# Kernel optimization log

Hardware: AMD Instinct MI355X
Metric: run time of the kernel (lower is better)

## Reference

```python
import jax, jax.numpy as jnp
import numpy as np

B, S, D = 8, 2048, 1024


def setup_inputs() -> dict:
    key = jax.random.key(0)
    ks = jax.random.split(key, 9)
    scale = 1.0 / np.sqrt(D)
    inp = {
        "query": jax.random.normal(ks[0], (B, S, D), dtype=jnp.float32),
        "key": jax.random.normal(ks[1], (B, S, D), dtype=jnp.float32),
        "value": jax.random.normal(ks[2], (B, S, D), dtype=jnp.float32),
        # causal boolean mask, broadcast over batch; True = keep, False = -inf
        "mask": jnp.tril(jnp.ones((S, S), dtype=bool)),
        "Wq": jax.random.normal(ks[3], (D, D), dtype=jnp.float32) * scale,
        "bq": jax.random.normal(ks[4], (D,), dtype=jnp.float32) * 0.02,
        "Wk": jax.random.normal(ks[5], (D, D), dtype=jnp.float32) * scale,
        "bk": jax.random.normal(ks[6], (D,), dtype=jnp.float32) * 0.02,
        "Wv": jax.random.normal(ks[7], (D, D), dtype=jnp.float32) * scale,
        "bv": jax.random.normal(ks[8], (D,), dtype=jnp.float32) * 0.02,
    }
    return inp


def reference(query, key, value, mask, Wq, bq, Wk, bk, Wv, bv):
    dk = Wq.shape[1]
    # linear projections: nn.Linear stores weight as [out,in]; here W is [in,out]
    q = jnp.einsum("bsd,de->bse", query, Wq) + bq
    k = jnp.einsum("bsd,de->bse", key, Wk) + bk
    v = jnp.einsum("bsd,de->bse", value, Wv) + bv
    # scaled dot-product scores [B, S, S]
    scores = jnp.einsum("bqd,bkd->bqk", q, k) / jnp.sqrt(jnp.asarray(dk, q.dtype))
    scores = jnp.where(mask, scores, jnp.asarray(-jnp.inf, scores.dtype))
    attn = jax.nn.softmax(scores, axis=-1)
    return jnp.einsum("bqk,bkd->bqd", attn, v)
```

## Files before the change

### kernel.cpp

```cpp
#include <hip/hip_runtime.h>

#define BB 8
#define SS 2048
#define DD 1024
#define BK 32
#define TSZ (128 * BK)

typedef unsigned short u16;
typedef __bf16 bf16x8 __attribute__((ext_vector_type(8)));
typedef float f32x4 __attribute__((ext_vector_type(4)));

__device__ __forceinline__ u16 f2bf(float f) {
  unsigned int u = __builtin_bit_cast(unsigned int, f);
  u += 0x7fffu + ((u >> 16) & 1u);
  return (u16)(u >> 16);
}
__device__ __forceinline__ float bf2f(u16 h) {
  unsigned int u = ((unsigned int)h) << 16;
  return __builtin_bit_cast(float, u);
}

__device__ __forceinline__ void gl2lds16(const u16* g, u16* l) {
  __builtin_amdgcn_global_load_lds(
      (const __attribute__((address_space(1))) unsigned int*)g,
      (__attribute__((address_space(3))) unsigned int*)l, 16, 0, 0);
}

__device__ __forceinline__ void stage_tile(const u16* gbase, size_t gstride,
                                           u16* lds, int wave, int lane) {
#pragma unroll
  for (int r = 0; r < 2; r++) {
    int rowblk = r * 64 + wave * 16;
    int row = rowblk + (lane >> 2);
    int col = (lane & 3) * 8;
    gl2lds16(gbase + (size_t)row * gstride + col, lds + rowblk * BK);
  }
}

__device__ __forceinline__ void mfma_tile(const u16* As, const u16* Bs, int wm, int wn,
                                          int quad, int l16, f32x4 (&acc)[4][4]) {
  bf16x8 a[4], b[4];
#pragma unroll
  for (int i = 0; i < 4; i++)
    a[i] = *reinterpret_cast<const bf16x8*>(&As[(wm + i * 16 + l16) * BK + quad * 8]);
#pragma unroll
  for (int j = 0; j < 4; j++)
    b[j] = *reinterpret_cast<const bf16x8*>(&Bs[(wn + j * 16 + l16) * BK + quad * 8]);
#pragma unroll
  for (int i = 0; i < 4; i++)
#pragma unroll
    for (int j = 0; j < 4; j++)
      acc[i][j] = __builtin_amdgcn_mfma_f32_16x16x32_bf16(a[i], b[j], acc[i][j], 0, 0, 0);
}

__global__ void prep(const float* __restrict__ q, const float* __restrict__ k,
                     const float* __restrict__ v, u16* __restrict__ Xall,
                     const float* __restrict__ Wq, const float* __restrict__ Wk,
                     const float* __restrict__ Wv, u16* __restrict__ Wall) {
  __shared__ u16 t[32][33];
  int id = blockIdx.x;
  if (id < 24576) {
    int z = id >> 13;
    int chunk = id & 8191;
    const float* x = (z == 0) ? q : (z == 1) ? k : v;
    u16* y = Xall + (size_t)z * (BB * SS * DD);
    size_t i = (size_t)chunk * 256 + threadIdx.x;
    const float4* s = (const float4*)x;
    float4 a = s[2 * i], b = s[2 * i + 1];
    uint4 p;
    p.x = (unsigned)f2bf(a.x) | ((unsigned)f2bf(a.y) << 16);
    p.y = (unsigned)f2bf(a.z) | ((unsigned)f2bf(a.w) << 16);
    p.z = (unsigned)f2bf(b.x) | ((unsigned)f2bf(b.y) << 16);
    p.w = (unsigned)f2bf(b.z) | ((unsigned)f2bf(b.w) << 16);
    ((uint4*)y)[i] = p;
  } else {
    int tt = id - 24576;
    int z = tt >> 10, t2 = tt & 1023;
    const float* W = (z == 0) ? Wq : (z == 1) ? Wk : Wv;
    u16* Wt = Wall + (size_t)z * (DD * DD);
    int n0 = (t2 & 31) * 32, k0 = (t2 >> 5) * 32;
    int tx = threadIdx.x & 31, ty = threadIdx.x >> 5;
#pragma unroll
    for (int i = 0; i < 32; i += 8)
      t[ty + i][tx] = f2bf(W[(size_t)(k0 + ty + i) * DD + n0 + tx]);
    __syncthreads();
#pragma unroll
    for (int i = 0; i < 32; i += 8)
      Wt[(size_t)(n0 + ty + i) * DD + k0 + tx] = t[tx][ty + i];
  }
}

__global__ void proj_gemm(const u16* __restrict__ Xall, const u16* __restrict__ Wall,
                          const float* __restrict__ bq, const float* __restrict__ bk,
                          const float* __restrict__ bv, u16* __restrict__ QK,
                          u16* __restrict__ Vt) {
  __shared__ __align__(16) u16 As[2 * TSZ];
  __shared__ __align__(16) u16 Bs[2 * TSZ];
  int id = blockIdx.x;
  int z = id >> 10, rem = id & 1023;
  int r = rem & 7, j = rem >> 3;
  int bn = j & 7, bm = ((j >> 3) << 3) | r;
  const u16* Xb = Xall + (size_t)z * (BB * SS * DD);
  const u16* Wt = Wall + (size_t)z * (DD * DD);
  const float* bias = (z == 0) ? bq : (z == 1) ? bk : bv;
  int m0 = bm * 128, n0 = bn * 128;
  int tid = threadIdx.x;
  int lane = tid & 63, wave = tid >> 6;
  int wm = (wave >> 1) * 64, wn = (wave & 1) * 64;
  int quad = lane >> 4, l16 = lane & 15;

  const u16* Abase = (z < 2) ? (Xb + (size_t)m0 * DD) : (Wt + (size_t)n0 * DD);
  const u16* Bbase = (z < 2) ? (Wt + (size_t)n0 * DD) : (Xb + (size_t)m0 * DD);

  f32x4 acc[4][4];
  f32x4 zz = {0.f, 0.f, 0.f, 0.f};
#pragma unroll
  for (int i = 0; i < 4; i++)
#pragma unroll
    for (int jj = 0; jj < 4; jj++) acc[i][jj] = zz;

  for (int k0 = 0; k0 < DD; k0 += 2 * BK) {
    __syncthreads();
    stage_tile(Abase + k0, DD, As, wave, lane);
    stage_tile(Abase + k0 + BK, DD, As + TSZ, wave, lane);
    stage_tile(Bbase + k0, DD, Bs, wave, lane);
    stage_tile(Bbase + k0 + BK, DD, Bs + TSZ, wave, lane);
    __syncthreads();
    mfma_tile(As, Bs, wm, wn, quad, l16, acc);
    mfma_tile(As + TSZ, Bs + TSZ, wm, wn, quad, l16, acc);
  }
  if (z < 2) {
    u16* Out = QK + (size_t)z * (BB * SS * DD);
#pragma unroll
    for (int i = 0; i < 4; i++) {
#pragma unroll
      for (int rr = 0; rr < 4; rr++) {
        int row = m0 + wm + i * 16 + quad * 4 + rr;
#pragma unroll
        for (int jj = 0; jj < 4; jj++) {
          int col = n0 + wn + jj * 16 + l16;
          Out[(size_t)row * DD + col] = f2bf(acc[i][jj][rr] + bias[col]);
        }
      }
    }
  } else {
    int b = m0 >> 11, s0 = m0 & 2047;
#pragma unroll
    for (int i = 0; i < 4; i++) {
#pragma unroll
      for (int rr = 0; rr < 4; rr++) {
        int d = n0 + wm + i * 16 + quad * 4 + rr;
        float bd = bias[d];
#pragma unroll
        for (int jj = 0; jj < 4; jj++) {
          int s = s0 + wn + jj * 16 + l16;
          Vt[((size_t)b * DD + d) * SS + s] = f2bf(acc[i][jj][rr] + bd);
        }
      }
    }
  }
}

__global__ void scores_gemm(const u16* __restrict__ Q, const u16* __restrict__ Kp,
                            u16* __restrict__ Sc) {
  __shared__ __align__(16) u16 As[2 * TSZ];
  __shared__ __align__(16) u16 Bs[2 * TSZ];
  int id = blockIdx.x;
  int b = id & 7, t = id >> 3;
  int bm = (int)((sqrtf(8.f * t + 1.f) - 1.f) * 0.5f);
  while ((bm + 1) * (bm + 2) / 2 <= t) bm++;
  while (bm * (bm + 1) / 2 > t) bm--;
  int bn = t - bm * (bm + 1) / 2;

  const u16* Qb = Q + (size_t)b * SS * DD;
  const u16* Kb = Kp + (size_t)b * SS * DD;
  u16* Sb = Sc + (size_t)b * SS * SS;
  int m0 = bm * 128, n0 = bn * 128;
  int tid = threadIdx.x;
  int lane = tid & 63, wave = tid >> 6;
  int wm = (wave >> 1) * 64, wn = (wave & 1) * 64;
  int quad = lane >> 4, l16 = lane & 15;

  f32x4 acc[4][4];
  f32x4 z = {0.f, 0.f, 0.f, 0.f};
#pragma unroll
  for (int i = 0; i < 4; i++)
#pragma unroll
    for (int jj = 0; jj < 4; jj++) acc[i][jj] = z;

  for (int k0 = 0; k0 < DD; k0 += 2 * BK) {
    __syncthreads();
    stage_tile(Qb + (size_t)m0 * DD + k0, DD, As, wave, lane);
    stage_tile(Qb + (size_t)m0 * DD + k0 + BK, DD, As + TSZ, wave, lane);
    stage_tile(Kb + (size_t)n0 * DD + k0, DD, Bs, wave, lane);
    stage_tile(Kb + (size_t)n0 * DD + k0 + BK, DD, Bs + TSZ, wave, lane);
    __syncthreads();
    mfma_tile(As, Bs, wm, wn, quad, l16, acc);
    mfma_tile(As + TSZ, Bs + TSZ, wm, wn, quad, l16, acc);
  }
#pragma unroll
  for (int i = 0; i < 4; i++) {
#pragma unroll
    for (int rr = 0; rr < 4; rr++) {
      int gi = m0 + wm + i * 16 + quad * 4 + rr;
#pragma unroll
      for (int jj = 0; jj < 4; jj++) {
        int gj = n0 + wn + jj * 16 + l16;
        if (gj <= gi) Sb[(size_t)gi * SS + gj] = f2bf(acc[i][jj][rr] * 0.03125f);
      }
    }
  }
}

__global__ void softmax_causal(const u16* __restrict__ Sc, u16* __restrict__ P) {
  int i = blockIdx.x, b = blockIdx.y;
  const u16* srow = Sc + ((size_t)b * SS + i) * SS;
  u16* prow = P + ((size_t)b * SS + i) * SS;
  int n = i + 1;
  int nceil = ((i >> 7) + 1) << 7;
  int tid = threadIdx.x;
  int lane = tid & 63, wave = tid >> 6;
  __shared__ float sm[4];
  __shared__ float ssum[4];

  int j0 = tid * 8;
  bool act = j0 < nceil;
  float v[8];
  float mx = -3.0e38f;
  if (act) {
    uint4 raw = ((const uint4*)srow)[tid];
    unsigned w[4] = {raw.x, raw.y, raw.z, raw.w};
#pragma unroll
    for (int u = 0; u < 8; u++) {
      u16 h = (u16)((w[u >> 1] >> ((u & 1) * 16)) & 0xffffu);
      v[u] = (j0 + u < n) ? bf2f(h) : -3.0e38f;
      mx = fmaxf(mx, v[u]);
    }
  } else {
#pragma unroll
    for (int u = 0; u < 8; u++) v[u] = -3.0e38f;
  }
#pragma unroll
  for (int off = 32; off > 0; off >>= 1) mx = fmaxf(mx, __shfl_down(mx, off, 64));
  if (lane == 0) sm[wave] = mx;
  __syncthreads();
  mx = fmaxf(fmaxf(sm[0], sm[1]), fmaxf(sm[2], sm[3]));

  float e[8];
  float sum = 0.f;
#pragma unroll
  for (int u = 0; u < 8; u++) {
    e[u] = __expf(v[u] - mx);
    sum += e[u];
  }
#pragma unroll
  for (int off = 32; off > 0; off >>= 1) sum += __shfl_down(sum, off, 64);
  if (lane == 0) ssum[wave] = sum;
  __syncthreads();
  sum = ssum[0] + ssum[1] + ssum[2] + ssum[3];
  float inv = 1.0f / sum;
  if (act) {
    uint4 o;
    unsigned* ow = (unsigned*)&o;
#pragma unroll
    for (int u = 0; u < 4; u++) {
      u16 lo = f2bf(e[2 * u] * inv);
      u16 hi = f2bf(e[2 * u + 1] * inv);
      ow[u] = (unsigned)lo | ((unsigned)hi << 16);
    }
    ((uint4*)prow)[tid] = o;
  }
}

__global__ void pv_gemm(const u16* __restrict__ P, const u16* __restrict__ Vt,
                        float* __restrict__ O) {
  __shared__ __align__(16) u16 As[2 * 64 * BK];
  __shared__ __align__(16) u16 Bs[2 * TSZ];
  int id = blockIdx.x;
  int bn = id & 7, q = (id >> 3) & 15, b = id >> 7;
  const u16* Pb = P + (size_t)b * SS * SS;
  const u16* Vb = Vt + (size_t)b * SS * DD;
  float* Ob = O + (size_t)b * SS * DD;
  int n0 = bn * 128;
  int tid = threadIdx.x;
  int lane = tid & 63, wave = tid >> 6;
  int wn = wave * 32;
  int quad = lane >> 4, l16 = lane & 15;

#pragma unroll
  for (int phase = 0; phase < 2; phase++) {
    int bm = phase ? (31 - q) : q;
    int m0 = bm * 64;
    f32x4 acc[4][2];
    f32x4 z = {0.f, 0.f, 0.f, 0.f};
#pragma unroll
    for (int i = 0; i < 4; i++)
#pragma unroll
      for (int jj = 0; jj < 2; jj++) acc[i][jj] = z;

    int kmax = (bm + 1) * 64;
    for (int k0 = 0; k0 < kmax; k0 += 2 * BK) {
      __syncthreads();
#pragma unroll
      for (int sub = 0; sub < 2; sub++) {
        int row = wave * 16 + (lane >> 2);
        int col = (lane & 3) * 8;
        gl2lds16(Pb + (size_t)(m0 + row) * SS + k0 + sub * BK + col,
                 As + sub * 64 * BK + wave * 16 * BK);
      }
      stage_tile(Vb + (size_t)n0 * SS + k0, SS, Bs, wave, lane);
      stage_tile(Vb + (size_t)n0 * SS + k0 + BK, SS, Bs + TSZ, wave, lane);
      __syncthreads();
#pragma unroll
      for (int sub = 0; sub < 2; sub++) {
        const u16* Asub = As + sub * 64 * BK;
        const u16* Bsub = Bs + sub * TSZ;
        bf16x8 a[4], bb[2];
#pragma unroll
        for (int i = 0; i < 4; i++)
          a[i] = *reinterpret_cast<const bf16x8*>(&Asub[(i * 16 + l16) * BK + quad * 8]);
#pragma unroll
        for (int jj = 0; jj < 2; jj++)
          bb[jj] = *reinterpret_cast<const bf16x8*>(&Bsub[(wn + jj * 16 + l16) * BK + quad * 8]);
#pragma unroll
        for (int i = 0; i < 4; i++)
#pragma unroll
          for (int jj = 0; jj < 2; jj++)
            acc[i][jj] = __builtin_amdgcn_mfma_f32_16x16x32_bf16(a[i], bb[jj], acc[i][jj], 0, 0, 0);
      }
    }
#pragma unroll
    for (int i = 0; i < 4; i++) {
#pragma unroll
      for (int rr = 0; rr < 4; rr++) {
        int row = m0 + i * 16 + quad * 4 + rr;
#pragma unroll
        for (int jj = 0; jj < 2; jj++) {
          int col = n0 + wn + jj * 16 + l16;
          Ob[(size_t)row * DD + col] = acc[i][jj][rr];
        }
      }
    }
  }
}

extern "C" void kernel_launch(void* const* d_in, const int* in_sizes, int n_in,
                              void* d_out, int out_size, void* d_ws, size_t ws_size,
                              hipStream_t stream) {
  const float* query = (const float*)d_in[0];
  const float* key_ = (const float*)d_in[1];
  const float* value = (const float*)d_in[2];
  const float* Wq = (const float*)d_in[4];
  const float* bq = (const float*)d_in[5];
  const float* Wk = (const float*)d_in[6];
  const float* bk = (const float*)d_in[7];
  const float* Wv = (const float*)d_in[8];
  const float* bv = (const float*)d_in[9];
  float* out = (float*)d_out;
  char* ws = (char*)d_ws;

  const size_t MB = 1048576ull;
  u16* Xall = (u16*)(ws + 0);
  u16* QK   = (u16*)(ws + 96 * MB);
  u16* Qb   = (u16*)(ws + 96 * MB);
  u16* Kb   = (u16*)(ws + 128 * MB);
  u16* Vt   = (u16*)(ws + 160 * MB);
  u16* Wall = (u16*)(ws + 192 * MB);
  u16* Sc   = (u16*)(ws + 32 * MB);
  u16* P    = (u16*)(ws + 96 * MB);

  dim3 blk(256, 1, 1);
  prep<<<dim3(27648, 1, 1), blk, 0, stream>>>(query, key_, value, Xall, Wq, Wk, Wv, Wall);
  proj_gemm<<<dim3(3072, 1, 1), blk, 0, stream>>>(Xall, Wall, bq, bk, bv, QK, Vt);
  scores_gemm<<<dim3(1088, 1, 1), blk, 0, stream>>>(Qb, Kb, Sc);
  softmax_causal<<<dim3(2048, 8, 1), blk, 0, stream>>>(Sc, P);
  pv_gemm<<<dim3(1024, 1, 1), blk, 0, stream>>>(P, Vt, out);
}
```

Baseline: 487.6 us.

## Rewrite projection GEMM with 256x256 tiles, 8 waves and pipelined LDS staging

The projection GEMM moves from 128x128 tiles with 4 waves to 256x256 tiles with 8 waves per block. It uses a deeper asynchronous global-to-LDS prefetch pipeline, throttled with explicit vmcnt waits and split barriers. LDS reads use an XOR swizzle to avoid bank conflicts, and the MFMA phases are interleaved with staging using setprio. The aim is higher operand reuse and less load latency exposed in the dominant GEMM stage, at the cost of more registers and LDS (128KB) and fragile hand-written synchronization.

```diff
diff --git a/kernel.cpp b/kernel.cpp
--- a/kernel.cpp
+++ b/kernel.cpp
@@ -90,70 +90,164 @@
   }
 }
 
-__global__ void proj_gemm(const u16* __restrict__ Xall, const u16* __restrict__ Wall,
-                          const float* __restrict__ bq, const float* __restrict__ bk,
-                          const float* __restrict__ bv, u16* __restrict__ QK,
-                          u16* __restrict__ Vt) {
-  __shared__ __align__(16) u16 As[2 * TSZ];
-  __shared__ __align__(16) u16 Bs[2 * TSZ];
+#define NKT 16
+
+#define LGK0 asm volatile("s_waitcnt lgkmcnt(0)" ::: "memory")
+#define VMW(n) asm volatile("s_waitcnt vmcnt(" #n ")" ::: "memory")
+#define BARF do { __builtin_amdgcn_s_barrier(); asm volatile("" ::: "memory"); } while (0)
+
+template <int I0, int J0>
+__device__ __forceinline__ void quad_mfma(f32x4 (&acc)[8][4], const bf16x8 (&a)[4][2],
+                                          const bf16x8 (&b)[2][2]) {
+#pragma unroll
+  for (int ks = 0; ks < 2; ks++)
+#pragma unroll
+    for (int i = 0; i < 4; i++)
+#pragma unroll
+      for (int jj = 0; jj < 2; jj++)
+        acc[I0 + i][J0 + jj] = __builtin_amdgcn_mfma_f32_16x16x32_bf16(
+            a[i][ks], b[jj][ks], acc[I0 + i][J0 + jj], 0, 0, 0);
+}
+
+__global__ __launch_bounds__(512, 2) void proj_gemm(
+    const u16* __restrict__ Xall, const u16* __restrict__ Wall,
+    const float* __restrict__ bq, const float* __restrict__ bk,
+    const float* __restrict__ bv, u16* __restrict__ QK, u16* __restrict__ Vt) {
+  __shared__ __align__(16) u16 sA[2][2][8192];
+  __shared__ __align__(16) u16 sB[2][2][8192];
   int id = blockIdx.x;
-  int z = id >> 10, rem = id & 1023;
-  int r = rem & 7, j = rem >> 3;
-  int bn = j & 7, bm = ((j >> 3) << 3) | r;
+  int z = id >> 8, rem = id & 255;
+  int r = rem & 7, j0 = rem >> 3;
+  int bw = j0 & 3, bx = (j0 >> 2) * 8 + r;
   const u16* Xb = Xall + (size_t)z * (BB * SS * DD);
   const u16* Wt = Wall + (size_t)z * (DD * DD);
   const float* bias = (z == 0) ? bq : (z == 1) ? bk : bv;
-  int m0 = bm * 128, n0 = bn * 128;
+  const u16* Ab = (z < 2) ? Xb + (size_t)bx * 256 * DD : Wt + (size_t)bw * 256 * DD;
+  const u16* Bb = (z < 2) ? Wt + (size_t)bw * 256 * DD : Xb + (size_t)bx * 256 * DD;
+
   int tid = threadIdx.x;
   int lane = tid & 63, wave = tid >> 6;
-  int wm = (wave >> 1) * 64, wn = (wave & 1) * 64;
-  int quad = lane >> 4, l16 = lane & 15;
-
-  const u16* Abase = (z < 2) ? (Xb + (size_t)m0 * DD) : (Wt + (size_t)n0 * DD);
-  const u16* Bbase = (z < 2) ? (Wt + (size_t)n0 * DD) : (Xb + (size_t)m0 * DD);
-
-  f32x4 acc[4][4];
+  int wrow = wave >> 2, wcol = wave & 3;
+  int quad = lane >> 4, l16 = lane & 15, sw = l16 & 7;
+  int k0off = (quad ^ sw) * 8;
+  int k1off = ((quad + 4) ^ sw) * 8;
+
+  u16* sAf = &sA[0][0][0];
+  u16* sBf = &sB[0][0][0];
+
+  auto stage = [&](int h) {
+    int tt = h >> 2, d = h & 3;
+    u16* l = ((d < 2) ? sBf : sAf) + ((((tt & 1) << 1) | (d & 1)) * 8192);
+    const u16* g = ((d < 2) ? Bb : Ab) + (size_t)((d & 1) * 128) * DD + tt * 64;
+#pragma unroll
+    for (int ii = 0; ii < 2; ii++) {
+      int reg = wave * 2 + ii;
+      int row = reg * 8 + (lane >> 3);
+      int col = ((lane & 7) ^ (lane >> 3)) * 8;
+      gl2lds16(g + (size_t)row * DD + col, l + reg * 512);
+    }
+  };
+
+  f32x4 acc[8][4];
   f32x4 zz = {0.f, 0.f, 0.f, 0.f};
 #pragma unroll
-  for (int i = 0; i < 4; i++)
+  for (int i = 0; i < 8; i++)
 #pragma unroll
     for (int jj = 0; jj < 4; jj++) acc[i][jj] = zz;
 
-  for (int k0 = 0; k0 < DD; k0 += 2 * BK) {
-    __syncthreads();
-    stage_tile(Abase + k0, DD, As, wave, lane);
-    stage_tile(Abase + k0 + BK, DD, As + TSZ, wave, lane);
-    stage_tile(Bbase + k0, DD, Bs, wave, lane);
-    stage_tile(Bbase + k0 + BK, DD, Bs + TSZ, wave, lane);
-    __syncthreads();
-    mfma_tile(As, Bs, wm, wn, quad, l16, acc);
-    mfma_tile(As + TSZ, Bs + TSZ, wm, wn, quad, l16, acc);
-  }
+#pragma unroll
+  for (int h = 0; h < 6; h++) stage(h);
+  VMW(4);
+  BARF;
+
+#pragma unroll 2
+  for (int t = 0; t < NKT; ++t) {
+    int buf = t & 1;
+    const u16* At0 = sAf + (buf * 2 + wrow) * 8192 + l16 * 64 + k0off;
+    const u16* At1 = sAf + (buf * 2 + wrow) * 8192 + l16 * 64 + k1off;
+    const u16* Bt0 = sBf + (buf * 2 + (wcol >> 1)) * 8192 + ((wcol & 1) * 64 + l16) * 64 + k0off;
+    const u16* Bt1 = sBf + (buf * 2 + (wcol >> 1)) * 8192 + ((wcol & 1) * 64 + l16) * 64 + k1off;
+    bf16x8 al[4][2], ah[4][2], bl[2][2], bh[2][2];
+#pragma unroll
+    for (int i = 0; i < 4; i++) {
+      al[i][0] = *reinterpret_cast<const bf16x8*>(At0 + i * 1024);
+      al[i][1] = *reinterpret_cast<const bf16x8*>(At1 + i * 1024);
+    }
+#pragma unroll
+    for (int jj = 0; jj < 2; jj++) {
+      bl[jj][0] = *reinterpret_cast<const bf16x8*>(Bt0 + jj * 1024);
+      bl[jj][1] = *reinterpret_cast<const bf16x8*>(Bt1 + jj * 1024);
+    }
+    if (4 * t + 6 < 4 * NKT) stage(4 * t + 6);
+    __builtin_amdgcn_s_barrier();
+    LGK0;
+    __builtin_amdgcn_s_setprio(1);
+    quad_mfma<0, 0>(acc, al, bl);
+    __builtin_amdgcn_s_setprio(0);
+    BARF;
+#pragma unroll
+    for (int jj = 0; jj < 2; jj++) {
+      bh[jj][0] = *reinterpret_cast<const bf16x8*>(Bt0 + (2 + jj) * 1024);
+      bh[jj][1] = *reinterpret_cast<const bf16x8*>(Bt1 + (2 + jj) * 1024);
+    }
+    if (4 * t + 7 < 4 * NKT) stage(4 * t + 7);
+    __builtin_amdgcn_s_barrier();
+    LGK0;
+    __builtin_amdgcn_s_setprio(1);
+    quad_mfma<0, 2>(acc, al, bh);
+    __builtin_amdgcn_s_setprio(0);
+    BARF;
+#pragma unroll
+    for (int i = 0; i < 4; i++) {
+      ah[i][0] = *reinterpret_cast<const bf16x8*>(At0 + (4 + i) * 1024);
+      ah[i][1] = *reinterpret_cast<const bf16x8*>(At1 + (4 + i) * 1024);
+    }
+    if (4 * t + 8 < 4 * NKT) stage(4 * t + 8);
+    __builtin_amdgcn_s_barrier();
+    LGK0;
+    __builtin_amdgcn_s_setprio(1);
+    quad_mfma<4, 0>(acc, ah, bl);
+    __builtin_amdgcn_s_setprio(0);
+    BARF;
+    if (4 * t + 9 < 4 * NKT) stage(4 * t + 9);
+    __builtin_amdgcn_s_barrier();
+    LGK0;
+    __builtin_amdgcn_s_setprio(1);
+    quad_mfma<4, 2>(acc, ah, bh);
+    __builtin_amdgcn_s_setprio(0);
+    if (t < NKT - 2) { VMW(4); } else if (t == NKT - 2) { VMW(0); }
+    BARF;
+  }
+
   if (z < 2) {
     u16* Out = QK + (size_t)z * (BB * SS * DD);
-#pragma unroll
-    for (int i = 0; i < 4; i++) {
+    int gm0 = bx * 256 + wrow * 128 + quad * 4;
+    int gn0 = bw * 256 + wcol * 64 + l16;
+#pragma unroll
+    for (int i = 0; i < 8; i++) {
 #pragma unroll
       for (int rr = 0; rr < 4; rr++) {
-        int row = m0 + wm + i * 16 + quad * 4 + rr;
+        int row = gm0 + i * 16 + rr;
 #pragma unroll
         for (int jj = 0; jj < 4; jj++) {
-          int col = n0 + wn + jj * 16 + l16;
+          int col = gn0 + jj * 16;
           Out[(size_t)row * DD + col] = f2bf(acc[i][jj][rr] + bias[col]);
         }
       }
     }
   } else {
-    int b = m0 >> 11, s0 = m0 & 2047;
-#pragma unroll
-    for (int i = 0; i < 4; i++) {
+    int b = bx >> 3;
+    int s0 = (bx & 7) * 256 + wcol * 64 + l16;
+    int d0 = bw * 256 + wrow * 128 + quad * 4;
+#pragma unroll
+    for (int i = 0; i < 8; i++) {
 #pragma unroll
       for (int rr = 0; rr < 4; rr++) {
-        int d = n0 + wm + i * 16 + quad * 4 + rr;
+        int d = d0 + i * 16 + rr;
         float bd = bias[d];
 #pragma unroll
         for (int jj = 0; jj < 4; jj++) {
-          int s = s0 + wn + jj * 16 + l16;
+          int s = s0 + jj * 16;
           Vt[((size_t)b * DD + d) * SS + s] = f2bf(acc[i][jj][rr] + bd);
         }
       }
@@ -371,7 +465,7 @@
 
   dim3 blk(256, 1, 1);
   prep<<<dim3(27648, 1, 1), blk, 0, stream>>>(query, key_, value, Xall, Wq, Wk, Wv, Wall);
-  proj_gemm<<<dim3(3072, 1, 1), blk, 0, stream>>>(Xall, Wall, bq, bk, bv, QK, Vt);
+  proj_gemm<<<dim3(768, 1, 1), dim3(512, 1, 1), 0, stream>>>(Xall, Wall, bq, bk, bv, QK, Vt);
   scores_gemm<<<dim3(1088, 1, 1), blk, 0, stream>>>(Qb, Kb, Sc);
   softmax_causal<<<dim3(2048, 8, 1), blk, 0, stream>>>(Sc, P);
   pv_gemm<<<dim3(1024, 1, 1), blk, 0, stream>>>(P, Vt, out);
```

Measured after the change: 468.6 us. 1.04x faster.
